# Kernel tuning notes

Measured on AMD Instinct MI355X. Metric: run time of the kernel, lower is better.

Reference implementation:

```python
import jax, jax.numpy as jnp
import numpy as np

N_NODES = 50000
N_EDGES = 800000
D = 64
NEG_SLOPE = 0.01  # torch F.leaky_relu default


def _gin_layer(h, src, dst, eps, W, b, activate):
    # max-aggregate neighbor features: for each dst node, max over incoming src feats
    msg = h[src]  # [E, D] gather
    agg = jax.ops.segment_max(msg, dst, num_segments=N_NODES)  # [N, D]
    # DGL fills nodes with no in-edges with 0 for max reduce
    agg = jnp.where(jnp.isfinite(agg), agg, jnp.zeros((), h.dtype))
    out = ((1.0 + eps) * h + agg) @ W + b
    if activate:
        out = jnp.where(out >= 0, out, NEG_SLOPE * out)
    return out


def setup_inputs() -> dict:
    key = jax.random.key(0)
    ks = jax.random.split(key, 6)
    scale = 1.0 / np.sqrt(D)
    return {
        "n_feat": jax.random.normal(ks[0], (N_NODES, D), dtype=jnp.float32),
        "W0": jax.random.normal(ks[1], (D, D), dtype=jnp.float32) * scale,
        "b0": jnp.zeros((D,), jnp.float32),
        "W1": jax.random.normal(ks[2], (D, D), dtype=jnp.float32) * scale,
        "b1": jnp.zeros((D,), jnp.float32),
        "W2": jax.random.normal(ks[3], (D, D), dtype=jnp.float32) * scale,
        "b2": jnp.zeros((D,), jnp.float32),
        "eps": jnp.zeros((3,), jnp.float32),
        "src": jax.random.randint(ks[4], (N_EDGES,), 0, N_NODES, dtype=jnp.int32),
        "dst": jax.random.randint(ks[5], (N_EDGES,), 0, N_NODES, dtype=jnp.int32),
    }


def reference(n_feat, W0, b0, W1, b1, W2, b2, eps, src, dst):
    h = _gin_layer(n_feat, src, dst, eps[0], W0, b0, activate=True)
    h = _gin_layer(h, src, dst, eps[1], W1, b1, activate=True)
    h = _gin_layer(h, src, dst, eps[2], W2, b2, activate=False)  # last_activate=False
    return h
```

## Files before the change

### kernel.cpp

```cpp
#include <hip/hip_runtime.h>

#define N_NODES 50000
#define N_EDGES 800000
#define D 64
#define CAP 64
#define XLD 72
#define SENT 50000

typedef short short8 __attribute__((ext_vector_type(8)));
typedef float floatx4 __attribute__((ext_vector_type(4)));
typedef unsigned short ushort_t;

__device__ __forceinline__ ushort_t f32_to_bf16(float f) {
    unsigned int u = __float_as_uint(f);
    u += 0x7FFFu + ((u >> 16) & 1u);
    return (ushort_t)(u >> 16);
}
__device__ __forceinline__ float bf16lo(unsigned int u) { return __uint_as_float(u << 16); }
__device__ __forceinline__ float bf16hi(unsigned int u) { return __uint_as_float(u & 0xFFFF0000u); }

__global__ void __launch_bounds__(256) prep_kernel(
        const float* __restrict__ in,
        ushort_t* __restrict__ hb0,
        ushort_t* __restrict__ hb1,
        const float* __restrict__ W0,
        const float* __restrict__ W1,
        const float* __restrict__ W2,
        ushort_t* __restrict__ wt_all,
        int* __restrict__ cnt,
        const int* __restrict__ src,
        const int* __restrict__ dst,
        ushort_t* __restrict__ bucket) {
    int b = blockIdx.x;
    if (b < 3125) {
        int t = b * 256 + threadIdx.x;
        float4 v = ((const float4*)in)[t];
        uint2 o;
        o.x = ((unsigned)f32_to_bf16(v.y) << 16) | f32_to_bf16(v.x);
        o.y = ((unsigned)f32_to_bf16(v.w) << 16) | f32_to_bf16(v.z);
        ((uint2*)hb0)[t] = o;
        if (b < 3) {
            const float* Ws[3] = {W0, W1, W2};
            const float* W = Ws[b];
            ushort_t* ow = wt_all + b * 4096;
            for (int idx = threadIdx.x; idx < 4096; idx += 256) {
                int k = idx >> 6, n = idx & 63;
                ow[n * 64 + k] = f32_to_bf16(W[idx]);
            }
            if (b == 0) {
                int l = threadIdx.x;
                if (l < 64) hb0[(size_t)SENT * 64 + l] = 0xFF80u;
                else if (l < 128) hb1[(size_t)SENT * 64 + (l - 64)] = 0xFF80u;
            }
        }
    } else {
        int e = (b - 3125) * 256 + threadIdx.x;
        int t = dst[e];
        int slot = atomicAdd(&cnt[t], 1);
        if (slot < CAP) bucket[t * CAP + slot] = (ushort_t)src[e];
    }
}

#define RED4(ua, ub, uc, ud)                                                                        \
    m0 = fmaxf(m0, fmaxf(fmaxf(bf16lo(ua.x), bf16lo(ub.x)), fmaxf(bf16lo(uc.x), bf16lo(ud.x))));    \
    m1 = fmaxf(m1, fmaxf(fmaxf(bf16hi(ua.x), bf16hi(ub.x)), fmaxf(bf16hi(uc.x), bf16hi(ud.x))));    \
    m2 = fmaxf(m2, fmaxf(fmaxf(bf16lo(ua.y), bf16lo(ub.y)), fmaxf(bf16lo(uc.y), bf16lo(ud.y))));    \
    m3 = fmaxf(m3, fmaxf(fmaxf(bf16hi(ua.y), bf16hi(ub.y)), fmaxf(bf16hi(uc.y), bf16hi(ud.y))));

__global__ void __launch_bounds__(256) layer_kernel(
        const ushort_t* __restrict__ hin,
        const int* __restrict__ cnt,
        const ushort_t* __restrict__ bucket,
        const ushort_t* __restrict__ wt,
        const float* __restrict__ bias,
        const float* __restrict__ eps_arr,
        int layer, int activate, int last,
        ushort_t* __restrict__ out_bf,
        float* __restrict__ out_f32) {
    __shared__ ushort_t bk[16 * CAP];
    __shared__ ushort_t xs[16 * XLD];

    const int tid = threadIdx.x;
    const int lane = tid & 63;
    const int wv = tid >> 6;
    const int grp = lane >> 4;
    const int l15 = lane & 15;
    const int fo = l15 * 4;
    const float ev = 1.0f + eps_arr[layer];

    const int r0 = blockIdx.x * 16 + wv * 4;

#pragma unroll
    for (int j = 0; j < 4; ++j)
        bk[(wv * 4 + j) * CAP + lane] = bucket[(r0 + j) * CAP + lane];

    const int rr = r0 + grp;
    const int cg = min(cnt[rr], CAP);
    int g0 = __builtin_amdgcn_readlane(cg, 0);
    int g1 = __builtin_amdgcn_readlane(cg, 16);
    int g2 = __builtin_amdgcn_readlane(cg, 32);
    int g3 = __builtin_amdgcn_readlane(cg, 48);
    const int cmax = (max(max(g0, g1), max(g2, g3)) + 15) & ~15;

    ushort_t* bkrow = &bk[(wv * 4 + grp) * CAP];
    for (int s = cg + l15; s < cmax; s += 16) bkrow[s] = (ushort_t)SENT;

    const uint2 sv = *(const uint2*)&hin[rr * 64 + fo];

    float m0 = -INFINITY, m1 = -INFINITY, m2 = -INFINITY, m3 = -INFINITY;
    for (int i = 0; i < cmax; i += 16) {
        ushort4 sa = *(const ushort4*)&bkrow[i];
        ushort4 sb = *(const ushort4*)&bkrow[i + 4];
        ushort4 sc = *(const ushort4*)&bkrow[i + 8];
        ushort4 sd = *(const ushort4*)&bkrow[i + 12];
        uint2 u0  = *(const uint2*)&hin[(int)sa.x * 64 + fo];
        uint2 u1  = *(const uint2*)&hin[(int)sa.y * 64 + fo];
        uint2 u2  = *(const uint2*)&hin[(int)sa.z * 64 + fo];
        uint2 u3  = *(const uint2*)&hin[(int)sa.w * 64 + fo];
        uint2 u4  = *(const uint2*)&hin[(int)sb.x * 64 + fo];
        uint2 u5  = *(const uint2*)&hin[(int)sb.y * 64 + fo];
        uint2 u6  = *(const uint2*)&hin[(int)sb.z * 64 + fo];
        uint2 u7  = *(const uint2*)&hin[(int)sb.w * 64 + fo];
        uint2 u8  = *(const uint2*)&hin[(int)sc.x * 64 + fo];
        uint2 u9  = *(const uint2*)&hin[(int)sc.y * 64 + fo];
        uint2 u10 = *(const uint2*)&hin[(int)sc.z * 64 + fo];
        uint2 u11 = *(const uint2*)&hin[(int)sc.w * 64 + fo];
        uint2 u12 = *(const uint2*)&hin[(int)sd.x * 64 + fo];
        uint2 u13 = *(const uint2*)&hin[(int)sd.y * 64 + fo];
        uint2 u14 = *(const uint2*)&hin[(int)sd.z * 64 + fo];
        uint2 u15 = *(const uint2*)&hin[(int)sd.w * 64 + fo];
        RED4(u0, u1, u2, u3)
        RED4(u4, u5, u6, u7)
        RED4(u8, u9, u10, u11)
        RED4(u12, u13, u14, u15)
    }
    float a0 = (cg > 0) ? m0 : 0.f, a1 = (cg > 0) ? m1 : 0.f;
    float a2 = (cg > 0) ? m2 : 0.f, a3 = (cg > 0) ? m3 : 0.f;
    float x0 = fmaf(ev, bf16lo(sv.x), a0), x1 = fmaf(ev, bf16hi(sv.x), a1);
    float x2 = fmaf(ev, bf16lo(sv.y), a2), x3 = fmaf(ev, bf16hi(sv.y), a3);
    uint2 w;
    w.x = ((unsigned)f32_to_bf16(x1) << 16) | f32_to_bf16(x0);
    w.y = ((unsigned)f32_to_bf16(x3) << 16) | f32_to_bf16(x2);
    *(uint2*)&xs[(wv * 4 + grp) * XLD + fo] = w;
    __syncthreads();

    const int hi = lane >> 4;
    const int kc = hi * 8;
    short8 fa0 = *(const short8*)&xs[l15 * XLD + kc];
    short8 fa1 = *(const short8*)&xs[l15 * XLD + 32 + kc];
    const int ncol = wv * 16 + l15;
    short8 fb0 = *(const short8*)&wt[ncol * 64 + kc];
    short8 fb1 = *(const short8*)&wt[ncol * 64 + 32 + kc];
    floatx4 acc = {0.f, 0.f, 0.f, 0.f};
    acc = __builtin_amdgcn_mfma_f32_16x16x32_bf16(fa0, fb0, acc, 0, 0, 0);
    acc = __builtin_amdgcn_mfma_f32_16x16x32_bf16(fa1, fb1, acc, 0, 0, 0);

    const float bv = bias[ncol];
#pragma unroll
    for (int i = 0; i < 4; ++i) {
        int grow = blockIdx.x * 16 + hi * 4 + i;
        float v = acc[i] + bv;
        if (activate) v = (v >= 0.f) ? v : 0.01f * v;
        if (last) out_f32[(size_t)grow * 64 + ncol] = v;
        else out_bf[(size_t)grow * 64 + ncol] = f32_to_bf16(v);
    }
}

extern "C" void kernel_launch(void* const* d_in, const int* in_sizes, int n_in,
                              void* d_out, int out_size, void* d_ws, size_t ws_size,
                              hipStream_t stream) {
    const float* n_feat = (const float*)d_in[0];
    const float* W0 = (const float*)d_in[1];
    const float* b0 = (const float*)d_in[2];
    const float* W1 = (const float*)d_in[3];
    const float* b1 = (const float*)d_in[4];
    const float* W2 = (const float*)d_in[5];
    const float* b2 = (const float*)d_in[6];
    const float* eps = (const float*)d_in[7];
    const int* src = (const int*)d_in[8];
    const int* dst = (const int*)d_in[9];
    float* out = (float*)d_out;

    const size_t BKT_OFF = 200192;
    const size_t HB0_OFF = BKT_OFF + (size_t)N_NODES * CAP * 2;
    const size_t HB1_OFF = HB0_OFF + (size_t)(N_NODES + 1) * 64 * 2;
    const size_t WT_OFF  = HB1_OFF + (size_t)(N_NODES + 1) * 64 * 2;

    int* cnt = (int*)d_ws;
    ushort_t* bucket = (ushort_t*)((char*)d_ws + BKT_OFF);
    ushort_t* hb0 = (ushort_t*)((char*)d_ws + HB0_OFF);
    ushort_t* hb1 = (ushort_t*)((char*)d_ws + HB1_OFF);
    ushort_t* wt_all = (ushort_t*)((char*)d_ws + WT_OFF);

    hipMemsetAsync(cnt, 0, (size_t)N_NODES * 4, stream);
    prep_kernel<<<6250, 256, 0, stream>>>(n_feat, hb0, hb1, W0, W1, W2, wt_all,
                                          cnt, src, dst, bucket);

    dim3 blk(256);
    layer_kernel<<<3125, blk, 0, stream>>>(hb0, cnt, bucket, wt_all,        b0, eps, 0, 1, 0, hb1, out);
    layer_kernel<<<3125, blk, 0, stream>>>(hb1, cnt, bucket, wt_all + 4096, b1, eps, 1, 1, 0, hb0, out);
    layer_kernel<<<3125, blk, 0, stream>>>(hb0, cnt, bucket, wt_all + 8192, b2, eps, 2, 0, 1, hb1, out);
}
```

Measured before the change: 202.8 us.

## Build CSR buckets via two-pass binned scatter with shared-memory local atomics

Replaces the per-edge global atomicAdd into per-node counters and scattered bucket writes with a two-stage build. Edges are first binned by dst>>8 into replicated per-bin buffers using few global atomics, then one block per bin assembles the 256-node buckets in shared memory and writes them out coalesced. The memset is dropped and counter zeroing moves into the conversion kernel. This adds two kernel launches and an extra pass over the edge list, and entries beyond the per-replica capacity are silently dropped. Bucket slot order also changes, which does not affect a max reduction.

After: 351.7 us. 1.73x slower.

```diff
diff --git a/kernel.cpp b/kernel.cpp
--- a/kernel.cpp
+++ b/kernel.cpp
@@ -6,6 +6,9 @@
 #define CAP 64
 #define XLD 72
 #define SENT 50000
+#define NBINS 196
+#define NREP 4
+#define REPCAP 1536
 
 typedef short short8 __attribute__((ext_vector_type(8)));
 typedef float floatx4 __attribute__((ext_vector_type(4)));
@@ -19,46 +22,94 @@
 __device__ __forceinline__ float bf16lo(unsigned int u) { return __uint_as_float(u << 16); }
 __device__ __forceinline__ float bf16hi(unsigned int u) { return __uint_as_float(u & 0xFFFF0000u); }
 
-__global__ void __launch_bounds__(256) prep_kernel(
-        const float* __restrict__ in,
-        ushort_t* __restrict__ hb0,
-        ushort_t* __restrict__ hb1,
-        const float* __restrict__ W0,
-        const float* __restrict__ W1,
-        const float* __restrict__ W2,
-        ushort_t* __restrict__ wt_all,
-        int* __restrict__ cnt,
-        const int* __restrict__ src,
-        const int* __restrict__ dst,
-        ushort_t* __restrict__ bucket) {
+__global__ void __launch_bounds__(256) cvtw_kernel(const float* __restrict__ in,
+                                                   ushort_t* __restrict__ hb0,
+                                                   ushort_t* __restrict__ hb1,
+                                                   const float* __restrict__ W0,
+                                                   const float* __restrict__ W1,
+                                                   const float* __restrict__ W2,
+                                                   ushort_t* __restrict__ wt_all,
+                                                   int* __restrict__ bin_cnt) {
     int b = blockIdx.x;
-    if (b < 3125) {
-        int t = b * 256 + threadIdx.x;
-        float4 v = ((const float4*)in)[t];
-        uint2 o;
-        o.x = ((unsigned)f32_to_bf16(v.y) << 16) | f32_to_bf16(v.x);
-        o.y = ((unsigned)f32_to_bf16(v.w) << 16) | f32_to_bf16(v.z);
-        ((uint2*)hb0)[t] = o;
-        if (b < 3) {
-            const float* Ws[3] = {W0, W1, W2};
-            const float* W = Ws[b];
-            ushort_t* ow = wt_all + b * 4096;
-            for (int idx = threadIdx.x; idx < 4096; idx += 256) {
-                int k = idx >> 6, n = idx & 63;
-                ow[n * 64 + k] = f32_to_bf16(W[idx]);
-            }
-            if (b == 0) {
-                int l = threadIdx.x;
-                if (l < 64) hb0[(size_t)SENT * 64 + l] = 0xFF80u;
-                else if (l < 128) hb1[(size_t)SENT * 64 + (l - 64)] = 0xFF80u;
-            }
+    int t = b * 256 + threadIdx.x;
+    float4 v = ((const float4*)in)[t];
+    uint2 o;
+    o.x = ((unsigned)f32_to_bf16(v.y) << 16) | f32_to_bf16(v.x);
+    o.y = ((unsigned)f32_to_bf16(v.w) << 16) | f32_to_bf16(v.z);
+    ((uint2*)hb0)[t] = o;
+    if (b < 3) {
+        const float* Ws[3] = {W0, W1, W2};
+        const float* W = Ws[b];
+        ushort_t* ow = wt_all + b * 4096;
+        for (int idx = threadIdx.x; idx < 4096; idx += 256) {
+            int k = idx >> 6, n = idx & 63;
+            ow[n * 64 + k] = f32_to_bf16(W[idx]);
         }
-    } else {
-        int e = (b - 3125) * 256 + threadIdx.x;
-        int t = dst[e];
-        int slot = atomicAdd(&cnt[t], 1);
-        if (slot < CAP) bucket[t * CAP + slot] = (ushort_t)src[e];
-    }
+        if (b == 0) {
+            int l = threadIdx.x;
+            if (l < 64) hb0[(size_t)SENT * 64 + l] = 0xFF80u;
+            else if (l < 128) hb1[(size_t)SENT * 64 + (l - 64)] = 0xFF80u;
+        }
+    } else if (b == 3) {
+#pragma unroll
+        for (int i = 0; i < NREP; ++i) bin_cnt[i * 256 + threadIdx.x] = 0;
+    }
+}
+
+__global__ void __launch_bounds__(256) binscatter_kernel(const int* __restrict__ src,
+                                                         const int* __restrict__ dst,
+                                                         int* __restrict__ bin_cnt,
+                                                         unsigned int* __restrict__ binbuf) {
+    int e = blockIdx.x * 256 + threadIdx.x;
+    int s = src[e];
+    int t = dst[e];
+    int bin = t >> 8;
+    int rep = threadIdx.x & (NREP - 1);
+    int pos = atomicAdd(&bin_cnt[rep * 256 + bin], 1);
+    if (pos < REPCAP)
+        binbuf[(size_t)bin * (NREP * REPCAP) + rep * REPCAP + pos] =
+            ((unsigned)(t & 255) << 16) | (unsigned)s;
+}
+
+__global__ void __launch_bounds__(256) binbuild_kernel(const int* __restrict__ bin_cnt,
+                                                       const unsigned int* __restrict__ binbuf,
+                                                       int* __restrict__ cnt,
+                                                       ushort_t* __restrict__ bucket) {
+    __shared__ int lcnt[256];
+    __shared__ ushort_t lbkt[256 * CAP];
+    const int tid = threadIdx.x;
+    const int bin = blockIdx.x;
+
+    lcnt[tid] = 0;
+    {
+        const unsigned int sp = ((unsigned)SENT << 16) | (unsigned)SENT;
+        uint4 s4 = {sp, sp, sp, sp};
+        uint4* lb4 = (uint4*)lbkt;
+#pragma unroll
+        for (int i = 0; i < 8; ++i) lb4[tid + 256 * i] = s4;
+    }
+    __syncthreads();
+
+    const unsigned int* buf = binbuf + (size_t)bin * (NREP * REPCAP);
+#pragma unroll 1
+    for (int rep = 0; rep < NREP; ++rep) {
+        int ne = min(bin_cnt[rep * 256 + bin], REPCAP);
+        const unsigned int* b = buf + rep * REPCAP;
+        for (int i = tid; i < ne; i += 256) {
+            unsigned int u = b[i];
+            int dlow = (u >> 16) & 255;
+            int slot = atomicAdd(&lcnt[dlow], 1);
+            if (slot < CAP) lbkt[dlow * CAP + slot] = (ushort_t)(u & 0xFFFFu);
+        }
+    }
+    __syncthreads();
+
+    const int nrows = min(256, N_NODES - bin * 256);
+    if (tid < nrows) cnt[bin * 256 + tid] = lcnt[tid];
+    const int nchunk = nrows * 8;
+    const uint4* lb4 = (const uint4*)lbkt;
+    uint4* gb4 = (uint4*)(bucket + (size_t)bin * 256 * CAP);
+    for (int i = tid; i < nchunk; i += 256) gb4[i] = lb4[i];
 }
 
 #define RED4(ua, ub, uc, ud)                                                                        \
@@ -181,20 +232,25 @@
     const int* dst = (const int*)d_in[9];
     float* out = (float*)d_out;
 
-    const size_t BKT_OFF = 200192;
-    const size_t HB0_OFF = BKT_OFF + (size_t)N_NODES * CAP * 2;
-    const size_t HB1_OFF = HB0_OFF + (size_t)(N_NODES + 1) * 64 * 2;
-    const size_t WT_OFF  = HB1_OFF + (size_t)(N_NODES + 1) * 64 * 2;
-
-    int* cnt = (int*)d_ws;
+    const size_t BINCNT_OFF = 0;
+    const size_t CNT_OFF    = 4096;
+    const size_t BKT_OFF    = 204288;
+    const size_t BINBUF_OFF = 6604288;
+    const size_t HB0_OFF    = 11421184;
+    const size_t HB1_OFF    = 17821312;
+    const size_t WT_OFF     = 24221440;
+
+    int* bin_cnt = (int*)((char*)d_ws + BINCNT_OFF);
+    int* cnt = (int*)((char*)d_ws + CNT_OFF);
     ushort_t* bucket = (ushort_t*)((char*)d_ws + BKT_OFF);
+    unsigned int* binbuf = (unsigned int*)((char*)d_ws + BINBUF_OFF);
     ushort_t* hb0 = (ushort_t*)((char*)d_ws + HB0_OFF);
     ushort_t* hb1 = (ushort_t*)((char*)d_ws + HB1_OFF);
     ushort_t* wt_all = (ushort_t*)((char*)d_ws + WT_OFF);
 
-    hipMemsetAsync(cnt, 0, (size_t)N_NODES * 4, stream);
-    prep_kernel<<<6250, 256, 0, stream>>>(n_feat, hb0, hb1, W0, W1, W2, wt_all,
-                                          cnt, src, dst, bucket);
+    cvtw_kernel<<<3125, 256, 0, stream>>>(n_feat, hb0, hb1, W0, W1, W2, wt_all, bin_cnt);
+    binscatter_kernel<<<3125, 256, 0, stream>>>(src, dst, bin_cnt, binbuf);
+    binbuild_kernel<<<NBINS, 256, 0, stream>>>(bin_cnt, binbuf, cnt, bucket);
 
     dim3 blk(256);
     layer_kernel<<<3125, blk, 0, stream>>>(hb0, cnt, bucket, wt_all,        b0, eps, 0, 1, 0, hb1, out);
```
